# Performance work log

Hardware: AMD Instinct MI355X
Metric: run time of the kernel (lower is better)

The kernel has to match this reference:

```python
import jax, jax.numpy as jnp
import numpy as np

N_NODES = 100000
N_EDGES = 1600000
DIM = 128


def setup_inputs() -> dict:
    key = jax.random.key(0)
    ks = jax.random.split(key, 8)
    s = 1.0 / np.sqrt(DIM)
    return {
        "x": jax.random.normal(ks[0], (N_NODES, DIM), dtype=jnp.float32),
        "edge_index": jax.random.randint(ks[1], (2, N_EDGES), 0, N_NODES, dtype=jnp.int64),
        "W1_l": jax.random.normal(ks[2], (DIM, DIM), dtype=jnp.float32) * s,
        "b1": jnp.zeros((DIM,), dtype=jnp.float32),
        "W1_r": jax.random.normal(ks[3], (DIM, DIM), dtype=jnp.float32) * s,
        "W2_l": jax.random.normal(ks[4], (DIM, DIM), dtype=jnp.float32) * s,
        "b2": jnp.zeros((DIM,), dtype=jnp.float32),
        "W2_r": jax.random.normal(ks[5], (DIM, DIM), dtype=jnp.float32) * s,
    }


def _sage_conv(h, src, dst, n, W_l, b, W_r):
    # mean aggregation of source-node features onto target nodes
    agg = jax.ops.segment_sum(h[src], dst, num_segments=n)          # [N, D]
    deg = jax.ops.segment_sum(jnp.ones_like(src, dtype=h.dtype), dst, num_segments=n)
    agg = agg / jnp.maximum(deg, 1.0)[:, None]
    # PyG SAGEConv: lin_l(aggr) + bias + lin_r(x)  (root weight, no bias on lin_r)
    return agg @ W_l + b + h @ W_r


def reference(x, edge_index, W1_l, b1, W1_r, W2_l, b2, W2_r):
    src, dst = edge_index[0], edge_index[1]
    n = x.shape[0]
    h = jax.nn.relu(_sage_conv(x, src, dst, n, W1_l, b1, W1_r))
    return _sage_conv(h, src, dst, n, W2_l, b2, W2_r)
```

## Files before the change

### kernel.cpp

```cpp
#include <hip/hip_runtime.h>

typedef unsigned short ushort_t;
typedef unsigned int uint_t;

typedef short bf16x8 __attribute__((ext_vector_type(8)));
typedef float f32x4 __attribute__((ext_vector_type(4)));

#define DIM 128
#define BSHIFT 8
#define BNODES 256
#define DBINS 64

__device__ __forceinline__ float bf2f(ushort_t u) {
    uint_t x = ((uint_t)u) << 16;
    float f;
    __builtin_memcpy(&f, &x, 4);
    return f;
}

__device__ __forceinline__ ushort_t f2bf(float f) {
    uint_t x;
    __builtin_memcpy(&x, &f, 4);
    uint_t r = (x + 0x7fffu + ((x >> 16) & 1u)) >> 16;
    return (ushort_t)r;
}


__global__ void k_cvt_f32_bf16(const float* __restrict__ in, ushort_t* __restrict__ out, int n4) {
    int i = blockIdx.x * blockDim.x + threadIdx.x;
    if (i < n4) {
        float4 f = ((const float4*)in)[i];
        ushort4 u;
        u.x = f2bf(f.x); u.y = f2bf(f.y); u.z = f2bf(f.z); u.w = f2bf(f.w);
        ((ushort4*)out)[i] = u;
    }
}

__global__ void k_wt4(const float* __restrict__ W0, const float* __restrict__ W1,
                      const float* __restrict__ W2, const float* __restrict__ W3,
                      ushort_t* __restrict__ T0, ushort_t* __restrict__ T1,
                      ushort_t* __restrict__ T2, ushort_t* __restrict__ T3) {
    int i = blockIdx.x * blockDim.x + threadIdx.x;
    int w = i >> 14, j = i & 16383;
    int n = j >> 7, k = j & 127;
    const float* W = (w == 0) ? W0 : (w == 1) ? W1 : (w == 2) ? W2 : W3;
    ushort_t* T = (w == 0) ? T0 : (w == 1) ? T1 : (w == 2) ? T2 : T3;
    T[j] = f2bf(W[k * DIM + n]);
}


__global__ __launch_bounds__(256) void k_bhist(const int* __restrict__ dst, int E, int NB,
                                               int* __restrict__ bucketCount) {
    __shared__ int hist[512];
    int t = threadIdx.x;
    for (int b = t; b < NB; b += 256) hist[b] = 0;
    __syncthreads();
    int per = (E + gridDim.x - 1) / gridDim.x;
    int beg = blockIdx.x * per, end = min(beg + per, E);
    for (int i = beg + t; i < end; i += 256)
        atomicAdd(&hist[dst[i] >> BSHIFT], 1);
    __syncthreads();
    for (int b = t; b < NB; b += 256) {
        int v = hist[b];
        if (v) atomicAdd(&bucketCount[b], v);
    }
}

__global__ __launch_bounds__(512) void k_bscan(const int* __restrict__ bucketCount, int NB, int E,
                                               int* __restrict__ bucketBase,
                                               int* __restrict__ bucketCursor,
                                               int* __restrict__ row_ptr, int N) {
    __shared__ int lds[512];
    int t = threadIdx.x;
    int v = (t < NB) ? bucketCount[t] : 0;
    lds[t] = v;
    __syncthreads();
    for (int off = 1; off < 512; off <<= 1) {
        int u = (t >= off) ? lds[t - off] : 0;
        __syncthreads();
        lds[t] += u;
        __syncthreads();
    }
    if (t < NB) {
        int b = lds[t] - v;
        bucketBase[t] = b;
        bucketCursor[t] = b;
    }
    if (t == 0) row_ptr[N] = E;
}

__global__ __launch_bounds__(256) void k_bucketize(const int* __restrict__ src,
                                                   const int* __restrict__ dst, int E, int NB,
                                                   int* __restrict__ bucketCursor,
                                                   uint_t* __restrict__ bebuf) {
    __shared__ int hist[512];
    __shared__ int base[512];
    int t = threadIdx.x;
    for (int b = t; b < NB; b += 256) hist[b] = 0;
    __syncthreads();
    int per = (E + gridDim.x - 1) / gridDim.x;
    int beg = blockIdx.x * per, end = min(beg + per, E);
    for (int i = beg + t; i < end; i += 256)
        atomicAdd(&hist[dst[i] >> BSHIFT], 1);
    __syncthreads();
    for (int b = t; b < NB; b += 256) {
        int v = hist[b];
        base[b] = v ? atomicAdd(&bucketCursor[b], v) : 0;
        hist[b] = 0;
    }
    __syncthreads();
    for (int i = beg + t; i < end; i += 256) {
        int d = dst[i], s = src[i];
        int b = d >> BSHIFT;
        int off = atomicAdd(&hist[b], 1);
        bebuf[base[b] + off] = ((uint_t)(d & (BNODES - 1)) << 24) | (uint_t)s;
    }
}

__global__ __launch_bounds__(256) void k_bcsr(const uint_t* __restrict__ bebuf,
                                              const int* __restrict__ bucketBase,
                                              const int* __restrict__ bucketCount, int N,
                                              int* __restrict__ row_ptr, int* __restrict__ csr) {
    __shared__ int hist[BNODES];
    __shared__ int cur[BNODES];
    int t = threadIdx.x;
    int b = blockIdx.x;
    int ebase = bucketBase[b], cnt = bucketCount[b];
    int nodeBase = b << BSHIFT;
    hist[t] = 0;
    __syncthreads();
    for (int i = t; i < cnt; i += 256)
        atomicAdd(&hist[bebuf[ebase + i] >> 24], 1);
    __syncthreads();
    int v = hist[t];
    for (int off = 1; off < 256; off <<= 1) {
        int u = (t >= off) ? hist[t - off] : 0;
        __syncthreads();
        hist[t] += u;
        __syncthreads();
    }
    int excl = hist[t] - v;
    int node = nodeBase + t;
    if (node < N) row_ptr[node] = ebase + excl;
    cur[t] = excl;
    __syncthreads();
    for (int i = t; i < cnt; i += 256) {
        uint_t e = bebuf[ebase + i];
        int dl = (int)(e >> 24);
        int pos = atomicAdd(&cur[dl], 1);
        csr[ebase + pos] = (int)(e & 0xFFFFFFu);
    }
}


__global__ __launch_bounds__(256) void k_dhist(const int* __restrict__ rp, int N,
                                               int* __restrict__ dhist) {
    __shared__ int h[DBINS];
    int t = threadIdx.x;
    if (t < DBINS) h[t] = 0;
    __syncthreads();
    int i = blockIdx.x * 256 + t;
    if (i < N) {
        int d = rp[i + 1] - rp[i];
        atomicAdd(&h[min(d, DBINS - 1)], 1);
    }
    __syncthreads();
    if (t < DBINS && h[t]) atomicAdd(&dhist[t], h[t]);
}

__global__ void k_dscan(const int* __restrict__ dhist, int* __restrict__ dcur) {
    __shared__ int l[DBINS];
    int t = threadIdx.x;
    int v = dhist[t];
    l[t] = v;
    __syncthreads();
    for (int off = 1; off < DBINS; off <<= 1) {
        int u = (t >= off) ? l[t - off] : 0;
        __syncthreads();
        l[t] += u;
        __syncthreads();
    }
    dcur[t] = l[t] - v;
}

__global__ __launch_bounds__(256) void k_dperm(const int* __restrict__ rp, int N,
                                               int* __restrict__ dcur, int* __restrict__ perm) {
    __shared__ int h[DBINS];
    __shared__ int base[DBINS];
    int t = threadIdx.x;
    if (t < DBINS) h[t] = 0;
    __syncthreads();
    int i = blockIdx.x * 256 + t;
    int b = -1;
    if (i < N) {
        int d = rp[i + 1] - rp[i];
        b = min(d, DBINS - 1);
        atomicAdd(&h[b], 1);
    }
    __syncthreads();
    if (t < DBINS) {
        int v = h[t];
        base[t] = v ? atomicAdd(&dcur[t], v) : 0;
        h[t] = 0;
    }
    __syncthreads();
    if (i < N) {
        int off = atomicAdd(&h[b], 1);
        perm[base[b] + off] = i;
    }
}


__device__ __forceinline__ void acc8(float* a, uint4 p) {
    a[0] += bf2f((ushort_t)(p.x & 0xffffu));
    a[1] += bf2f((ushort_t)(p.x >> 16));
    a[2] += bf2f((ushort_t)(p.y & 0xffffu));
    a[3] += bf2f((ushort_t)(p.y >> 16));
    a[4] += bf2f((ushort_t)(p.z & 0xffffu));
    a[5] += bf2f((ushort_t)(p.z >> 16));
    a[6] += bf2f((ushort_t)(p.w & 0xffffu));
    a[7] += bf2f((ushort_t)(p.w >> 16));
}

__global__ __launch_bounds__(256) void k_agg(const ushort_t* __restrict__ X,
                                             const int* __restrict__ row_ptr,
                                             const int* __restrict__ csr,
                                             const int* __restrict__ perm,
                                             ushort_t* __restrict__ out, int n) {
    int g = (int)((blockIdx.x * (unsigned)blockDim.x + threadIdx.x) >> 4);
    if (g >= n) return;
    int node = perm[g];
    int sl = threadIdx.x & 15;
    int beg = row_ptr[node], end = row_ptr[node + 1];
    float a[8] = {0.f, 0.f, 0.f, 0.f, 0.f, 0.f, 0.f, 0.f};

    int e = beg;
    for (; e + 4 <= end; e += 4) {
        int s0 = csr[e + 0], s1 = csr[e + 1], s2 = csr[e + 2], s3 = csr[e + 3];
        uint4 p0 = *(const uint4*)(X + (size_t)s0 * DIM + sl * 8);
        uint4 p1 = *(const uint4*)(X + (size_t)s1 * DIM + sl * 8);
        uint4 p2 = *(const uint4*)(X + (size_t)s2 * DIM + sl * 8);
        uint4 p3 = *(const uint4*)(X + (size_t)s3 * DIM + sl * 8);
        acc8(a, p0); acc8(a, p1); acc8(a, p2); acc8(a, p3);
    }
    for (; e < end; e++) {
        int s = csr[e];
        uint4 p = *(const uint4*)(X + (size_t)s * DIM + sl * 8);
        acc8(a, p);
    }

    int cnt = end - beg;
    float sc = (cnt > 0) ? 1.f / (float)cnt : 0.f;
    uint4 o;
    o.x = (uint_t)f2bf(a[0] * sc) | ((uint_t)f2bf(a[1] * sc) << 16);
    o.y = (uint_t)f2bf(a[2] * sc) | ((uint_t)f2bf(a[3] * sc) << 16);
    o.z = (uint_t)f2bf(a[4] * sc) | ((uint_t)f2bf(a[5] * sc) << 16);
    o.w = (uint_t)f2bf(a[6] * sc) | ((uint_t)f2bf(a[7] * sc) << 16);
    *(uint4*)(out + (size_t)node * DIM + sl * 8) = o;
}


template <bool RELU, bool OUT_BF16>
__global__ __launch_bounds__(256) void k_gemm(const ushort_t* __restrict__ A1,
                                              const ushort_t* __restrict__ A2,
                                              const ushort_t* __restrict__ WTl,
                                              const ushort_t* __restrict__ WTr,
                                              const float* __restrict__ bias,
                                              void* __restrict__ Out, int n_waves, int M) {
    __shared__ ushort_t sW[2 * 128 * 128];
    int t = threadIdx.x;
    int wave = (int)((blockIdx.x * 256u + t) >> 6);
    int lane = t & 63;
    int col = lane & 15;
    int quad = lane >> 4;
    bool active = (wave < n_waves);

    bf16x8 a[2][8];
    if (active) {
#pragma unroll
        for (int tt = 0; tt < 2; tt++) {
            int arow = wave * 32 + tt * 16 + col;
            const ushort_t* a1p = A1 + (size_t)arow * DIM + quad * 8;
            const ushort_t* a2p = A2 + (size_t)arow * DIM + quad * 8;
#pragma unroll
            for (int ks = 0; ks < 4; ks++) a[tt][ks] = *(const bf16x8*)(a1p + ks * 32);
#pragma unroll
            for (int ks = 0; ks < 4; ks++) a[tt][4 + ks] = *(const bf16x8*)(a2p + ks * 32);
        }
    }

    {
        int tab = t >> 7, row = t & 127;
        const ushort_t* g = (tab ? WTr : WTl) + (size_t)row * 128;
        ushort_t* d = sW + (size_t)t * 128;
        int sw = row & 15;
#pragma unroll
        for (int c = 0; c < 16; c++) {
            uint4 v = *(const uint4*)(g + c * 8);
            *(uint4*)(d + ((c ^ sw) * 8)) = v;
        }
    }
    __syncthreads();
    if (!active) return;

    f32x4 acc[2][8];
#pragma unroll
    for (int tt = 0; tt < 2; tt++)
#pragma unroll
        for (int nt = 0; nt < 8; nt++) acc[tt][nt] = (f32x4){0.f, 0.f, 0.f, 0.f};

    const ushort_t* sWl = sW;
    const ushort_t* sWr = sW + 128 * 128;
#pragma unroll
    for (int nt = 0; nt < 8; nt++) {
        int row = nt * 16 + col;
        const ushort_t* bl = sWl + (size_t)row * 128;
        const ushort_t* br = sWr + (size_t)row * 128;
#pragma unroll
        for (int ks = 0; ks < 4; ks++) {
            bf16x8 b = *(const bf16x8*)(bl + (((ks * 4 + quad) ^ col) * 8));
            acc[0][nt] = __builtin_amdgcn_mfma_f32_16x16x32_bf16(a[0][ks], b, acc[0][nt], 0, 0, 0);
            acc[1][nt] = __builtin_amdgcn_mfma_f32_16x16x32_bf16(a[1][ks], b, acc[1][nt], 0, 0, 0);
        }
#pragma unroll
        for (int ks = 0; ks < 4; ks++) {
            bf16x8 b = *(const bf16x8*)(br + (((ks * 4 + quad) ^ col) * 8));
            acc[0][nt] = __builtin_amdgcn_mfma_f32_16x16x32_bf16(a[0][4 + ks], b, acc[0][nt], 0, 0, 0);
            acc[1][nt] = __builtin_amdgcn_mfma_f32_16x16x32_bf16(a[1][4 + ks], b, acc[1][nt], 0, 0, 0);
        }
    }

#pragma unroll
    for (int tt = 0; tt < 2; tt++)
#pragma unroll
        for (int nt = 0; nt < 8; nt++) {
            int c = nt * 16 + col;
            float bv = bias[c];
#pragma unroll
            for (int r = 0; r < 4; r++) {
                int m = wave * 32 + tt * 16 + quad * 4 + r;
                if (m < M) {
                    float v = acc[tt][nt][r] + bv;
                    if (RELU) v = v > 0.f ? v : 0.f;
                    if (OUT_BF16)
                        ((ushort_t*)Out)[(size_t)m * DIM + c] = f2bf(v);
                    else
                        ((float*)Out)[(size_t)m * DIM + c] = v;
                }
            }
        }
}


extern "C" void kernel_launch(void* const* d_in, const int* in_sizes, int n_in,
                              void* d_out, int out_size, void* d_ws, size_t ws_size,
                              hipStream_t stream) {
    const int N = in_sizes[0] / DIM;
    const int E = in_sizes[1] / 2;
    const int NB = (N + BNODES - 1) >> BSHIFT;

    const float* x   = (const float*)d_in[0];
    const int*   ei  = (const int*)d_in[1];
    const int*   src = ei;
    const int*   dst = ei + E;
    const float* W1l = (const float*)d_in[2];
    const float* b1  = (const float*)d_in[3];
    const float* W1r = (const float*)d_in[4];
    const float* W2l = (const float*)d_in[5];
    const float* b2  = (const float*)d_in[6];
    const float* W2r = (const float*)d_in[7];
    float* out = (float*)d_out;

    char* ws = (char*)d_ws;
    size_t off = 0;
    auto alloc = [&](size_t bytes) -> char* {
        char* p = ws + off;
        off = (off + bytes + 255) & ~(size_t)255;
        return p;
    };

    int*      bucketCount  = (int*)alloc((size_t)NB * 4);
    int*      dhist        = (int*)alloc((size_t)DBINS * 4);
    int*      dcur         = (int*)alloc((size_t)DBINS * 4);
    int*      bucketBase   = (int*)alloc((size_t)NB * 4);
    int*      bucketCursor = (int*)alloc((size_t)NB * 4);
    int*      row_ptr      = (int*)alloc((size_t)(N + 1) * 4);
    int*      csr          = (int*)alloc((size_t)E * 4);
    uint_t*   bebuf        = (uint_t*)alloc((size_t)E * 4);
    size_t    fpad         = (size_t)32 * DIM * 2;
    ushort_t* xb           = (ushort_t*)alloc((size_t)N * DIM * 2 + fpad);
    ushort_t* hb           = (ushort_t*)alloc((size_t)N * DIM * 2 + fpad);
    ushort_t* aggb         = (ushort_t*)alloc((size_t)N * DIM * 2 + fpad);
    ushort_t* wt1l         = (ushort_t*)alloc((size_t)DIM * DIM * 2);
    ushort_t* wt1r         = (ushort_t*)alloc((size_t)DIM * DIM * 2);
    ushort_t* wt2l         = (ushort_t*)alloc((size_t)DIM * DIM * 2);
    ushort_t* wt2r         = (ushort_t*)alloc((size_t)DIM * DIM * 2);
    int*      perm         = (int*)bebuf;

    hipMemsetAsync(bucketCount, 0, (size_t)((char*)dhist - (char*)bucketCount) + DBINS * 4, stream);

    {
        int n4 = N * DIM / 4;
        k_cvt_f32_bf16<<<dim3((n4 + 255) / 256), dim3(256), 0, stream>>>(x, xb, n4);
    }
    k_wt4<<<dim3(4 * DIM * DIM / 256), dim3(256), 0, stream>>>(W1l, W1r, W2l, W2r,
                                                               wt1l, wt1r, wt2l, wt2r);
    k_bhist<<<dim3(256), dim3(256), 0, stream>>>(dst, E, NB, bucketCount);
    k_bscan<<<dim3(1), dim3(512), 0, stream>>>(bucketCount, NB, E, bucketBase, bucketCursor, row_ptr, N);
    k_bucketize<<<dim3(256), dim3(256), 0, stream>>>(src, dst, E, NB, bucketCursor, bebuf);
    k_bcsr<<<dim3(NB), dim3(256), 0, stream>>>(bebuf, bucketBase, bucketCount, N, row_ptr, csr);

    const int nblk = (N + 255) / 256;
    k_dhist<<<dim3(nblk), dim3(256), 0, stream>>>(row_ptr, N, dhist);
    k_dscan<<<dim3(1), dim3(DBINS), 0, stream>>>(dhist, dcur);
    k_dperm<<<dim3(nblk), dim3(256), 0, stream>>>(row_ptr, N, dcur, perm);

    const int n_waves = (N + 31) / 32;
    dim3 gemm_grid((n_waves + 3) / 4), gemm_blk(256);
    dim3 agg_grid((N + 15) / 16), agg_blk(256);

    k_agg<<<agg_grid, agg_blk, 0, stream>>>(xb, row_ptr, csr, perm, aggb, N);
    k_gemm<true, true><<<gemm_grid, gemm_blk, 0, stream>>>(aggb, xb, wt1l, wt1r, b1, hb, n_waves, N);
    k_agg<<<agg_grid, agg_blk, 0, stream>>>(hb, row_ptr, csr, perm, aggb, N);
    k_gemm<false, false><<<gemm_grid, gemm_blk, 0, stream>>>(aggb, hb, wt2l, wt2r, b2, out, n_waves, N);

    (void)n_in; (void)out_size; (void)ws_size;
}
```

Measured before the change: 375.0 us.

## Fuse prep kernels, fold degree histogram into CSR build, deepen gather unroll

Merges the feature conversion and weight transpose into a single launch, and computes the degree histogram inside the CSR build kernel so the separate histogram kernel is gone. The aggregation loop now issues 8 independent row loads per iteration before accumulating, and bf16-to-float unpacking uses shifts and masks directly. The aim is fewer launches and more memory-level parallelism in the gather, at the cost of somewhat higher register pressure in the aggregation kernel.

```diff
diff --git a/kernel.cpp b/kernel.cpp
--- a/kernel.cpp
+++ b/kernel.cpp
@@ -26,26 +26,28 @@
 }
 
 
-__global__ void k_cvt_f32_bf16(const float* __restrict__ in, ushort_t* __restrict__ out, int n4) {
-    int i = blockIdx.x * blockDim.x + threadIdx.x;
+__global__ __launch_bounds__(256) void k_prep(const float* __restrict__ x, ushort_t* __restrict__ xb,
+                                              int n4,
+                                              const float* __restrict__ W0, const float* __restrict__ W1,
+                                              const float* __restrict__ W2, const float* __restrict__ W3,
+                                              ushort_t* __restrict__ T0, ushort_t* __restrict__ T1,
+                                              ushort_t* __restrict__ T2, ushort_t* __restrict__ T3) {
+    int i = blockIdx.x * 256 + threadIdx.x;
     if (i < n4) {
-        float4 f = ((const float4*)in)[i];
+        float4 f = ((const float4*)x)[i];
         ushort4 u;
         u.x = f2bf(f.x); u.y = f2bf(f.y); u.z = f2bf(f.z); u.w = f2bf(f.w);
-        ((ushort4*)out)[i] = u;
-    }
-}
-
-__global__ void k_wt4(const float* __restrict__ W0, const float* __restrict__ W1,
-                      const float* __restrict__ W2, const float* __restrict__ W3,
-                      ushort_t* __restrict__ T0, ushort_t* __restrict__ T1,
-                      ushort_t* __restrict__ T2, ushort_t* __restrict__ T3) {
-    int i = blockIdx.x * blockDim.x + threadIdx.x;
-    int w = i >> 14, j = i & 16383;
-    int n = j >> 7, k = j & 127;
-    const float* W = (w == 0) ? W0 : (w == 1) ? W1 : (w == 2) ? W2 : W3;
-    ushort_t* T = (w == 0) ? T0 : (w == 1) ? T1 : (w == 2) ? T2 : T3;
-    T[j] = f2bf(W[k * DIM + n]);
+        ((ushort4*)xb)[i] = u;
+    } else {
+        int j = i - n4;
+        if (j < 4 * DIM * DIM) {
+            int w = j >> 14; j &= 16383;
+            int n = j >> 7, k = j & 127;
+            const float* W = (w == 0) ? W0 : (w == 1) ? W1 : (w == 2) ? W2 : W3;
+            ushort_t* T = (w == 0) ? T0 : (w == 1) ? T1 : (w == 2) ? T2 : T3;
+            T[j] = f2bf(W[k * DIM + n]);
+        }
+    }
 }
 
 
@@ -120,19 +122,24 @@
 __global__ __launch_bounds__(256) void k_bcsr(const uint_t* __restrict__ bebuf,
                                               const int* __restrict__ bucketBase,
                                               const int* __restrict__ bucketCount, int N,
-                                              int* __restrict__ row_ptr, int* __restrict__ csr) {
+                                              int* __restrict__ row_ptr, int* __restrict__ csr,
+                                              int* __restrict__ dhist) {
     __shared__ int hist[BNODES];
     __shared__ int cur[BNODES];
+    __shared__ int dh[DBINS];
     int t = threadIdx.x;
     int b = blockIdx.x;
     int ebase = bucketBase[b], cnt = bucketCount[b];
     int nodeBase = b << BSHIFT;
     hist[t] = 0;
+    if (t < DBINS) dh[t] = 0;
     __syncthreads();
     for (int i = t; i < cnt; i += 256)
         atomicAdd(&hist[bebuf[ebase + i] >> 24], 1);
     __syncthreads();
     int v = hist[t];
+    int node = nodeBase + t;
+    if (node < N) atomicAdd(&dh[min(v, DBINS - 1)], 1);
     for (int off = 1; off < 256; off <<= 1) {
         int u = (t >= off) ? hist[t - off] : 0;
         __syncthreads();
@@ -140,7 +147,6 @@
         __syncthreads();
     }
     int excl = hist[t] - v;
-    int node = nodeBase + t;
     if (node < N) row_ptr[node] = ebase + excl;
     cur[t] = excl;
     __syncthreads();
@@ -150,23 +156,13 @@
         int pos = atomicAdd(&cur[dl], 1);
         csr[ebase + pos] = (int)(e & 0xFFFFFFu);
     }
-}
-
-
-__global__ __launch_bounds__(256) void k_dhist(const int* __restrict__ rp, int N,
-                                               int* __restrict__ dhist) {
-    __shared__ int h[DBINS];
-    int t = threadIdx.x;
-    if (t < DBINS) h[t] = 0;
-    __syncthreads();
-    int i = blockIdx.x * 256 + t;
-    if (i < N) {
-        int d = rp[i + 1] - rp[i];
-        atomicAdd(&h[min(d, DBINS - 1)], 1);
-    }
-    __syncthreads();
-    if (t < DBINS && h[t]) atomicAdd(&dhist[t], h[t]);
-}
+    __syncthreads();
+    if (t < DBINS) {
+        int c = dh[t];
+        if (c) atomicAdd(&dhist[t], c);
+    }
+}
+
 
 __global__ void k_dscan(const int* __restrict__ dhist, int* __restrict__ dcur) {
     __shared__ int l[DBINS];
@@ -212,14 +208,15 @@
 
 
 __device__ __forceinline__ void acc8(float* a, uint4 p) {
-    a[0] += bf2f((ushort_t)(p.x & 0xffffu));
-    a[1] += bf2f((ushort_t)(p.x >> 16));
-    a[2] += bf2f((ushort_t)(p.y & 0xffffu));
-    a[3] += bf2f((ushort_t)(p.y >> 16));
-    a[4] += bf2f((ushort_t)(p.z & 0xffffu));
-    a[5] += bf2f((ushort_t)(p.z >> 16));
-    a[6] += bf2f((ushort_t)(p.w & 0xffffu));
-    a[7] += bf2f((ushort_t)(p.w >> 16));
+    union { uint_t u; float f; } c;
+    c.u = p.x << 16;         a[0] += c.f;
+    c.u = p.x & 0xffff0000u; a[1] += c.f;
+    c.u = p.y << 16;         a[2] += c.f;
+    c.u = p.y & 0xffff0000u; a[3] += c.f;
+    c.u = p.z << 16;         a[4] += c.f;
+    c.u = p.z & 0xffff0000u; a[5] += c.f;
+    c.u = p.w << 16;         a[6] += c.f;
+    c.u = p.w & 0xffff0000u; a[7] += c.f;
 }
 
 __global__ __launch_bounds__(256) void k_agg(const ushort_t* __restrict__ X,
@@ -235,13 +232,26 @@
     float a[8] = {0.f, 0.f, 0.f, 0.f, 0.f, 0.f, 0.f, 0.f};
 
     int e = beg;
-    for (; e + 4 <= end; e += 4) {
-        int s0 = csr[e + 0], s1 = csr[e + 1], s2 = csr[e + 2], s3 = csr[e + 3];
-        uint4 p0 = *(const uint4*)(X + (size_t)s0 * DIM + sl * 8);
-        uint4 p1 = *(const uint4*)(X + (size_t)s1 * DIM + sl * 8);
-        uint4 p2 = *(const uint4*)(X + (size_t)s2 * DIM + sl * 8);
-        uint4 p3 = *(const uint4*)(X + (size_t)s3 * DIM + sl * 8);
-        acc8(a, p0); acc8(a, p1); acc8(a, p2); acc8(a, p3);
+    for (; e + 8 <= end; e += 8) {
+        uint4 p[8];
+#pragma unroll
+        for (int j = 0; j < 8; j++) {
+            int s = csr[e + j];
+            p[j] = *(const uint4*)(X + (size_t)s * DIM + sl * 8);
+        }
+#pragma unroll
+        for (int j = 0; j < 8; j++) acc8(a, p[j]);
+    }
+    if (e + 4 <= end) {
+        uint4 p[4];
+#pragma unroll
+        for (int j = 0; j < 4; j++) {
+            int s = csr[e + j];
+            p[j] = *(const uint4*)(X + (size_t)s * DIM + sl * 8);
+        }
+#pragma unroll
+        for (int j = 0; j < 4; j++) acc8(a, p[j]);
+        e += 4;
     }
     for (; e < end; e++) {
         int s = csr[e];
@@ -401,17 +411,16 @@
 
     {
         int n4 = N * DIM / 4;
-        k_cvt_f32_bf16<<<dim3((n4 + 255) / 256), dim3(256), 0, stream>>>(x, xb, n4);
-    }
-    k_wt4<<<dim3(4 * DIM * DIM / 256), dim3(256), 0, stream>>>(W1l, W1r, W2l, W2r,
-                                                               wt1l, wt1r, wt2l, wt2r);
+        int total = n4 + 4 * DIM * DIM;
+        k_prep<<<dim3((total + 255) / 256), dim3(256), 0, stream>>>(
+            x, xb, n4, W1l, W1r, W2l, W2r, wt1l, wt1r, wt2l, wt2r);
+    }
     k_bhist<<<dim3(256), dim3(256), 0, stream>>>(dst, E, NB, bucketCount);
     k_bscan<<<dim3(1), dim3(512), 0, stream>>>(bucketCount, NB, E, bucketBase, bucketCursor, row_ptr, N);
     k_bucketize<<<dim3(256), dim3(256), 0, stream>>>(src, dst, E, NB, bucketCursor, bebuf);
-    k_bcsr<<<dim3(NB), dim3(256), 0, stream>>>(bebuf, bucketBase, bucketCount, N, row_ptr, csr);
+    k_bcsr<<<dim3(NB), dim3(256), 0, stream>>>(bebuf, bucketBase, bucketCount, N, row_ptr, csr, dhist);
 
     const int nblk = (N + 255) / 256;
-    k_dhist<<<dim3(nblk), dim3(256), 0, stream>>>(row_ptr, N, dhist);
     k_dscan<<<dim3(1), dim3(DBINS), 0, stream>>>(dhist, dcur);
     k_dperm<<<dim3(nblk), dim3(256), 0, stream>>>(row_ptr, N, dcur, perm);
 
```

After: 367.1 us. 1.02x faster.
